# Performance work log

Measured on AMD Instinct MI355X. Metric: run time of the kernel, lower is better.

Reference implementation:

```python
import jax, jax.numpy as jnp
import numpy as np

N, D, H, B = 16384, 256, 4, 64
K_EDGE, TOP_K, NUM_HOPS = 3, 5, 2
EDGE_THRESH = 0.3
EPS = 1e-8


def setup_inputs() -> dict:
    key = jax.random.key(0)
    ks = jax.random.split(key, 32)
    g = lambda i, shape, sc=1.0: jax.random.normal(ks[i], shape, jnp.float32) * sc
    # sparse-ish symmetric adjacency (avg ~33 nonzeros/row, like a pruned memory graph)
    adj = jax.random.uniform(ks[0], (N, N), jnp.float32)
    adj = adj * (jax.random.uniform(ks[1], (N, N), jnp.float32) < 0.002)
    adj = jnp.maximum(adj, adj.T)
    return dict(
        nodes=g(2, (N, D)),
        node_values=g(3, (N,)),
        adjacency=adj,
        related_pos=g(4, (B, D)),
        query=g(5, (B, D)),
        w_in=g(6, (3 * D, D), D ** -0.5),
        b_in=jnp.zeros((3 * D,), jnp.float32),
        w_out=g(7, (D, D), D ** -0.5),
        b_out=jnp.zeros((D,), jnp.float32),
        rel_w1=g(8, (2 * D, D), (2 * D) ** -0.5),
        rel_b1=jnp.zeros((D,), jnp.float32),
        rel_w2=g(9, (D, D // 2), D ** -0.5),
        rel_b2=jnp.zeros((D // 2,), jnp.float32),
        rel_w3=g(10, (D // 2, 1), (D // 2) ** -0.5),
        rel_b3=jnp.zeros((1,), jnp.float32),
        gru_w_ih=g(11, (3 * D, D), D ** -0.5),
        gru_w_hh=g(12, (3 * D, D), D ** -0.5),
        gru_b_ih=jnp.zeros((3 * D,), jnp.float32),
        gru_b_hh=jnp.zeros((3 * D,), jnp.float32),
        node_timestamps=jax.random.randint(ks[13], (N,), 0, N),
        write_idx=jax.random.randint(ks[14], (B,), 0, N),
        total_writes=N,
    )


def _l2n(x):
    return x / (jnp.linalg.norm(x, axis=-1, keepdims=True) + EPS)


def reference(nodes, node_values, adjacency, related_pos, query,
              w_in, b_in, w_out, b_out,
              rel_w1, rel_b1, rel_w2, rel_b2, rel_w3, rel_b3,
              gru_w_ih, gru_w_hh, gru_b_ih, gru_b_hh,
              node_timestamps, write_idx, total_writes):
    b, d = query.shape
    n = nodes.shape[0]
    dh = d // H
    nodes_n = _l2n(nodes)

    # ---- write path: cosine-sim top-k edge scoring + relation-encoder MLP ----
    sims_w = _l2n(related_pos) @ nodes_n.T                      # [B,N]
    _, nbr = jax.lax.top_k(sims_w, K_EDGE)                      # [B,K]
    src = nodes[write_idx]                                      # [B,D]
    dst = nodes[nbr]                                            # [B,K,D]
    comb = jnp.concatenate(
        [jnp.broadcast_to(src[:, None, :], dst.shape), dst], -1)  # [B,K,2D]
    h = jax.nn.relu(comb @ rel_w1 + rel_b1)
    h = jax.nn.relu(h @ rel_w2 + rel_b2)
    strength = jax.nn.sigmoid(h @ rel_w3 + rel_b3)[..., 0]     # [B,K]
    same = nbr == write_idx[:, None]
    old = adjacency[write_idx[:, None], nbr]
    val = jnp.where(same, old, strength)                        # skip self-edges
    adj2 = adjacency.at[write_idx[:, None], nbr].set(val)
    adj2 = adj2.at[nbr, write_idx[:, None]].set(val)            # symmetric write

    # ---- retrieval: weighted cosine similarity + top-k seeds ----
    sims = _l2n(query) @ nodes_n.T                              # [B,N]
    recency = jnp.exp(-0.01 * (total_writes - node_timestamps).astype(jnp.float32))
    weighted = sims * jax.nn.sigmoid(node_values) * recency
    _, seed = jax.lax.top_k(weighted, TOP_K)                    # [B,TOP_K]
    visited = jnp.zeros((b, n), bool).at[jnp.arange(b)[:, None], seed].set(True)

    # ---- multi-hop graph expansion over thresholded adjacency ----
    adj_bool = (adj2 > EDGE_THRESH).astype(jnp.float32)
    for _ in range(NUM_HOPS):
        visited = visited | ((visited.astype(jnp.float32) @ adj_bool) > 0)

    # ---- masked multi-head attention: query attends to visited nodes ----
    q = (query @ w_in[:d].T + b_in[:d]).reshape(b, H, dh)
    k = (nodes @ w_in[d:2 * d].T + b_in[d:2 * d]).reshape(n, H, dh)
    v = (nodes @ w_in[2 * d:].T + b_in[2 * d:]).reshape(n, H, dh)
    scores = jnp.einsum('bhd,nhd->bhn', q, k) / np.float32(np.sqrt(dh))
    scores = jnp.where(visited[:, None, :], scores, jnp.float32(-1e9))
    attn = jax.nn.softmax(scores, axis=-1)
    ctx = jnp.einsum('bhn,nhd->bhd', attn, v).reshape(b, d)
    attended = ctx @ w_out.T + b_out                            # [B,D]

    # ---- GRUCell memory evolution: x=query, h=attended ----
    gi = query @ gru_w_ih.T + gru_b_ih
    gh = attended @ gru_w_hh.T + gru_b_hh
    i_r, i_z, i_n = jnp.split(gi, 3, -1)
    h_r, h_z, h_n = jnp.split(gh, 3, -1)
    r = jax.nn.sigmoid(i_r + h_r)
    z = jax.nn.sigmoid(i_z + h_z)
    nn_ = jnp.tanh(i_n + r * h_n)
    evolved = (1.0 - z) * nn_ + z * attended                    # [B,D]
    return evolved
```

## Files before the change

kernel.cpp:

```cpp
#include <hip/hip_runtime.h>
#include <math.h>
#include <stdint.h>

#define NN 16384
#define DD 256
#define ETH 0.3f
#define EDGE_CAP (4*1024*1024)

typedef unsigned long long u64;
typedef uint32_t u32;
typedef float f32x4 __attribute__((ext_vector_type(4)));

__global__ __launch_bounds__(256) void node_stats_k(const float* __restrict__ nodes,
    const float* __restrict__ nv, const int* __restrict__ ts, const int* __restrict__ tw,
    float* __restrict__ inv_norm, float* __restrict__ sal){
  int row = blockIdx.x*4 + (threadIdx.x>>6);
  int lane = threadIdx.x & 63;
  const float4* r4 = (const float4*)(nodes + (size_t)row*DD);
  float4 v = r4[lane];
  float s = v.x*v.x+v.y*v.y+v.z*v.z+v.w*v.w;
  #pragma unroll
  for (int o=32;o>0;o>>=1) s += __shfl_down(s,o);
  if (lane==0){
    inv_norm[row] = 1.0f/(sqrtf(s)+1e-8f);
    float x = nv[row];
    float sig = 1.0f/(1.0f+expf(-x));
    float rec = expf(-0.01f*(float)(tw[0]-ts[row]));
    sal[row] = sig*rec;
  }
}

__global__ __launch_bounds__(64) void norm_qr_k(const float* __restrict__ query,
    const float* __restrict__ related, float* __restrict__ qr){
  int blk = blockIdx.x; int lane = threadIdx.x;
  const float* src = (blk<64)? (related + (size_t)blk*DD) : (query + (size_t)(blk-64)*DD);
  float4 v = ((const float4*)src)[lane];
  float s = v.x*v.x+v.y*v.y+v.z*v.z+v.w*v.w;
  #pragma unroll
  for (int o=32;o>0;o>>=1) s += __shfl_down(s,o);
  s = __shfl(s,0);
  float inv = 1.0f/(sqrtf(s)+1e-8f);
  ((float4*)(qr + (size_t)blk*DD))[lane] = make_float4(v.x*inv,v.y*inv,v.z*inv,v.w*inv);
}

#define ACC8(r) do{ \
    accA[r].x += qs*nv0.x; accA[r].y += qs*nv0.y; accA[r].z += qs*nv0.z; accA[r].w += qs*nv0.w; \
    accB[r].x += qs*nv1.x; accB[r].y += qs*nv1.y; accB[r].z += qs*nv1.z; accB[r].w += qs*nv1.w; }while(0)

template<int RM>
__global__ __launch_bounds__(256) void gemm_smallM_k(const float* __restrict__ Qm,
    const float* __restrict__ nodes, float* __restrict__ out0, float* __restrict__ out1,
    const float* __restrict__ inv_norm, const float* __restrict__ sal, int mode){
  constexpr int M = RM*32;
  constexpr int KC = 32;
  __shared__ float qk[KC*M];
  __shared__ float ndk[KC*64];
  int t = threadIdx.x;
  int qg = t>>3, ng = t&7;
  int n0 = blockIdx.x*64;
  float4 accA[RM], accB[RM];
  #pragma unroll
  for (int r=0;r<RM;r++){ accA[r]=make_float4(0,0,0,0); accB[r]=make_float4(0,0,0,0); }
  for (int kb=0; kb<DD; kb+=KC){
    if (t < M){
      const float4* src = (const float4*)(Qm + (size_t)t*DD + kb);
      #pragma unroll
      for (int i=0;i<KC/4;i++){
        float4 w = src[i];
        qk[(i*4+0)*M+t]=w.x; qk[(i*4+1)*M+t]=w.y;
        qk[(i*4+2)*M+t]=w.z; qk[(i*4+3)*M+t]=w.w;
      }
    }
    {
      int nn = t&63, kq = t>>6;
      const float4* src = (const float4*)(nodes + (size_t)(n0+nn)*DD + kb + kq*8);
      float4 a = src[0], b = src[1];
      ndk[(kq*8+0)*64+nn]=a.x; ndk[(kq*8+1)*64+nn]=a.y; ndk[(kq*8+2)*64+nn]=a.z; ndk[(kq*8+3)*64+nn]=a.w;
      ndk[(kq*8+4)*64+nn]=b.x; ndk[(kq*8+5)*64+nn]=b.y; ndk[(kq*8+6)*64+nn]=b.z; ndk[(kq*8+7)*64+nn]=b.w;
    }
    __syncthreads();
    for (int k=0;k<KC;k++){
      float4 nv0 = *(const float4*)&ndk[k*64 + ng*8];
      float4 nv1 = *(const float4*)&ndk[k*64 + ng*8 + 4];
      float4 q0  = *(const float4*)&qk[k*M + qg*RM];
      float qs;
      qs=q0.x; ACC8(0); qs=q0.y; ACC8(1); qs=q0.z; ACC8(2); qs=q0.w; ACC8(3);
      if constexpr (RM==8){
        float4 q1 = *(const float4*)&qk[k*M + qg*RM + 4];
        qs=q1.x; ACC8(4); qs=q1.y; ACC8(5); qs=q1.z; ACC8(6); qs=q1.w; ACC8(7);
      }
    }
    __syncthreads();
  }
  int nbase = n0 + ng*8;
  float4 in0, in1, sa0, sa1;
  if (mode==0){
    in0 = *(const float4*)&inv_norm[nbase]; in1 = *(const float4*)&inv_norm[nbase+4];
    sa0 = *(const float4*)&sal[nbase];      sa1 = *(const float4*)&sal[nbase+4];
  }
  #pragma unroll
  for (int r=0;r<RM;r++){
    int row = qg*RM + r;
    float4 a = accA[r], b = accB[r];
    if (mode==0){
      float4 s0 = make_float4(a.x*in0.x, a.y*in0.y, a.z*in0.z, a.w*in0.w);
      float4 s1 = make_float4(b.x*in1.x, b.y*in1.y, b.z*in1.z, b.w*in1.w);
      if (row < 64){
        *(float4*)&out0[(size_t)row*NN + nbase]     = s0;
        *(float4*)&out0[(size_t)row*NN + nbase + 4] = s1;
      } else {
        float4 w0 = make_float4(s0.x*sa0.x, s0.y*sa0.y, s0.z*sa0.z, s0.w*sa0.w);
        float4 w1 = make_float4(s1.x*sa1.x, s1.y*sa1.y, s1.z*sa1.z, s1.w*sa1.w);
        *(float4*)&out1[(size_t)(row-64)*NN + nbase]     = w0;
        *(float4*)&out1[(size_t)(row-64)*NN + nbase + 4] = w1;
      }
    } else {
      float4 s0 = make_float4(a.x*0.125f, a.y*0.125f, a.z*0.125f, a.w*0.125f);
      float4 s1 = make_float4(b.x*0.125f, b.y*0.125f, b.z*0.125f, b.w*0.125f);
      *(float4*)&out0[(size_t)row*NN + nbase]     = s0;
      *(float4*)&out0[(size_t)row*NN + nbase + 4] = s1;
    }
  }
}

__global__ __launch_bounds__(1024) void topk_k(const float* __restrict__ src, int K,
    int* __restrict__ outIdx, u64* __restrict__ vis){
  int b = blockIdx.x, t = threadIdx.x;
  const float* row = src + (size_t)b*NN;
  __shared__ float sv[1024]; __shared__ int si[1024]; __shared__ int chosen[5];
  for (int kk=0;kk<K;kk++){
    float best = -3.0e38f; int bi = NN;
    for (int n=t;n<NN;n+=1024){
      bool skip=false;
      for (int c=0;c<kk;c++) if (chosen[c]==n) skip=true;
      if (skip) continue;
      float v = row[n];
      if (v > best){ best=v; bi=n; }
    }
    sv[t]=best; si[t]=bi;
    __syncthreads();
    for (int s=512;s>0;s>>=1){
      if (t<s){
        float v2=sv[t+s]; int i2=si[t+s];
        if (v2>sv[t] || (v2==sv[t] && i2<si[t])){ sv[t]=v2; si[t]=i2; }
      }
      __syncthreads();
    }
    if (t==0){
      chosen[kk]=si[0]; outIdx[b*K+kk]=si[0];
      if (vis) atomicOr(&vis[si[0]], 1ull<<b);
    }
    __syncthreads();
  }
}

__global__ __launch_bounds__(256) void rel_patch_k(const float* __restrict__ nodes,
    const int* __restrict__ write_idx, const int* __restrict__ nbr,
    const float* __restrict__ w1, const float* __restrict__ b1,
    const float* __restrict__ w2, const float* __restrict__ b2,
    const float* __restrict__ w3, const float* __restrict__ b3,
    u32* __restrict__ modkeys, u32* __restrict__ addkeys, int* __restrict__ ctrl,
    u32* __restrict__ rowmod){
  int b = blockIdx.x, t = threadIdx.x;
  __shared__ float comb[512], h1[256], red[128];
  int w = write_idx[b];
  for (int k=0;k<3;k++){
    int nb = nbr[b*3+k];
    comb[t]     = nodes[(size_t)w*DD + t];
    comb[256+t] = nodes[(size_t)nb*DD + t];
    __syncthreads();
    float a1 = b1[t];
    for (int i=0;i<512;i++) a1 += comb[i]*w1[(size_t)i*256 + t];
    h1[t] = a1>0.f ? a1 : 0.f;
    __syncthreads();
    if (t<128){
      float a2 = b2[t];
      for (int i=0;i<256;i++) a2 += h1[i]*w2[(size_t)i*128 + t];
      float h2 = a2>0.f ? a2 : 0.f;
      red[t] = h2*w3[t];
    }
    __syncthreads();
    for (int s=64;s>0;s>>=1){ if (t<s) red[t]+=red[t+s]; __syncthreads(); }
    if (t==0 && nb != w){
      float strength = 1.0f/(1.0f+expf(-(red[0]+b3[0])));
      u32 k1 = ((u32)w<<14)|(u32)nb, k2 = ((u32)nb<<14)|(u32)w;
      int m = atomicAdd(&ctrl[1],2);
      modkeys[m]=k1; modkeys[m+1]=k2;
      if (strength > ETH){ int a=atomicAdd(&ctrl[2],2); addkeys[a]=k1; addkeys[a+1]=k2; }
      atomicOr(&rowmod[(u32)w>>5], 1u<<((u32)w&31));
      atomicOr(&rowmod[(u32)nb>>5], 1u<<((u32)nb&31));
    }
    __syncthreads();
  }
}

#define LCAP 4096
#define GITER 8
#define ISSUE(P, GB) do{ \
  asm volatile("global_load_dwordx4 %0, %1, off" : "=v"(P##0) : "v"(a4 + tid + (size_t)((GB)+0)*stride)); \
  asm volatile("global_load_dwordx4 %0, %1, off" : "=v"(P##1) : "v"(a4 + tid + (size_t)((GB)+1)*stride)); \
  asm volatile("global_load_dwordx4 %0, %1, off" : "=v"(P##2) : "v"(a4 + tid + (size_t)((GB)+2)*stride)); \
  asm volatile("global_load_dwordx4 %0, %1, off" : "=v"(P##3) : "v"(a4 + tid + (size_t)((GB)+3)*stride)); \
  asm volatile("global_load_dwordx4 %0, %1, off" : "=v"(P##4) : "v"(a4 + tid + (size_t)((GB)+4)*stride)); \
  asm volatile("global_load_dwordx4 %0, %1, off" : "=v"(P##5) : "v"(a4 + tid + (size_t)((GB)+5)*stride)); \
  asm volatile("global_load_dwordx4 %0, %1, off" : "=v"(P##6) : "v"(a4 + tid + (size_t)((GB)+6)*stride)); \
  asm volatile("global_load_dwordx4 %0, %1, off" : "=v"(P##7) : "v"(a4 + tid + (size_t)((GB)+7)*stride)); \
}while(0)
#define PROC1(XX, GI) do{ \
  _Pragma("unroll") \
  for (int e=0;e<4;e++){ \
    if (XX[e] > ETH){ \
      size_t li = (tid + (size_t)(GI)*stride)*4 + e; \
      u32 i = (u32)(li >> 14), j = (u32)(li & 16383); \
      u32 key = (i<<14)|j; \
      bool keep = true; \
      if ((rowmod[i>>5]>>(i&31))&1u){ \
        for (int c=0;c<nm;c++) if (modkeys[c]==key){ keep=false; break; } \
      } \
      if (keep){ \
        int p = atomicAdd(&lcnt, 1); \
        if (p < LCAP) lbuf[p] = key; \
        else { int d = atomicAdd(ecnt,1); if (d < EDGE_CAP) edges[d] = key; } \
      } \
    } \
  } }while(0)
#define PROC8(P, GB) do{ \
  PROC1(P##0,(GB)+0); PROC1(P##1,(GB)+1); PROC1(P##2,(GB)+2); PROC1(P##3,(GB)+3); \
  PROC1(P##4,(GB)+4); PROC1(P##5,(GB)+5); PROC1(P##6,(GB)+6); PROC1(P##7,(GB)+7); \
}while(0)

__global__ __launch_bounds__(256) void scan_adj_k(const float* __restrict__ adj,
    const u32* __restrict__ rowmod, const u32* __restrict__ modkeys,
    const int* __restrict__ ctrl, u32* __restrict__ edges, int* __restrict__ ecnt){
  __shared__ u32 lbuf[LCAP];
  __shared__ int lcnt, gbase;
  int t = threadIdx.x;
  if (t==0) lcnt = 0;
  __syncthreads();
  int nm = ctrl[1];
  size_t tid = (size_t)blockIdx.x*256 + t;
  size_t stride = (size_t)gridDim.x*256;
  const f32x4* a4 = (const f32x4*)adj;
  const size_t total4 = (size_t)NN*NN/4;
  const int iters = (int)(total4 / stride);
  f32x4 xa0,xa1,xa2,xa3,xa4,xa5,xa6,xa7;
  f32x4 xb0,xb1,xb2,xb3,xb4,xb5,xb6,xb7;
  ISSUE(xa, 0);
  #pragma unroll 1
  for (int g=0; g<iters; g+=2*GITER){
    ISSUE(xb, g+GITER);
    asm volatile("s_waitcnt vmcnt(8)" ::: "memory");
    __builtin_amdgcn_sched_barrier(0);
    PROC8(xa, g);
    if (g + 2*GITER < iters){
      ISSUE(xa, g+2*GITER);
      asm volatile("s_waitcnt vmcnt(8)" ::: "memory");
    } else {
      asm volatile("s_waitcnt vmcnt(0)" ::: "memory");
    }
    __builtin_amdgcn_sched_barrier(0);
    PROC8(xb, g+GITER);
  }
  __syncthreads();
  int cnt = lcnt; if (cnt > LCAP) cnt = LCAP;
  if (cnt > 0){
    if (t==0) gbase = atomicAdd(ecnt, cnt);
    __syncthreads();
    int b0 = gbase;
    for (int i=t; i<cnt; i+=256){
      int d = b0 + i;
      if (d < EDGE_CAP) edges[d] = lbuf[i];
    }
  }
}

__global__ void patch_add_k(const u32* __restrict__ addkeys, const int* __restrict__ ctrl,
    u32* __restrict__ edges, int* __restrict__ ecnt){
  if (blockIdx.x==0 && threadIdx.x==0){
    int na = ctrl[2];
    int base = atomicAdd(ecnt, na);
    for (int i=0;i<na;i++) if (base+i < EDGE_CAP) edges[base+i] = addkeys[i];
  }
}

__global__ __launch_bounds__(256) void propagate_k(const u32* __restrict__ edges,
    const int* __restrict__ ecnt, const u64* __restrict__ vin, u64* __restrict__ vout){
  int n = *ecnt; if (n > EDGE_CAP) n = EDGE_CAP;
  int tid = blockIdx.x*256 + threadIdx.x;
  int stride = gridDim.x*256;
  for (int idx=tid; idx<n; idx+=stride){
    u32 key = edges[idx];
    u32 i = key>>14, j = key & 16383u;
    u64 wv = vin[i];
    if (wv) atomicOr(&vout[j], wv);
  }
}

__global__ __launch_bounds__(256) void qproj_k(const float* __restrict__ query,
    const float* __restrict__ w_in, const float* __restrict__ b_in, float* __restrict__ qproj){
  int b = blockIdx.x, o = threadIdx.x;
  float s = b_in[o];
  const float* wr = w_in + (size_t)o*256;
  const float* q = query + (size_t)b*256;
  for (int c=0;c<256;c++) s += q[c]*wr[c];
  qproj[b*256+o]=s;
}

__global__ __launch_bounds__(256) void qw_k(const float* __restrict__ qproj,
    const float* __restrict__ w_in, float* __restrict__ qW){
  int r = blockIdx.x;
  int c = threadIdx.x;
  int b = r>>2, hh = r&3;
  float s=0.f;
  for (int dh=0; dh<64; dh++)
    s += qproj[b*256 + hh*64 + dh] * w_in[(size_t)(256 + hh*64 + dh)*256 + c];
  qW[(size_t)r*256+c]=s;
}

__global__ __launch_bounds__(256) void rowstat_k(const float* __restrict__ scores,
    const u64* __restrict__ vis, float* __restrict__ m_out, float* __restrict__ is_out){
  int r = blockIdx.x; int bb = r >> 2; int t = threadIdx.x;
  const float* row = scores + (size_t)r*NN;
  float m = -3.0e38f, s = 0.f;
  for (int n=t; n<NN; n+=256){
    if ((vis[n]>>bb)&1ull){
      float v = row[n];
      if (v > m){ s = s*__expf(m - v) + 1.0f; m = v; }
      else s += __expf(v - m);
    }
  }
  __shared__ float sm[256], ss[256];
  sm[t]=m; ss[t]=s; __syncthreads();
  for (int st=128; st>0; st>>=1){
    if (t<st){
      float m2=sm[t+st], s2=ss[t+st];
      float mm = fmaxf(sm[t], m2);
      ss[t] = ss[t]*__expf(sm[t]-mm) + s2*__expf(m2-mm);
      sm[t] = mm;
    }
    __syncthreads();
  }
  if (t==0){ m_out[r] = sm[0]; is_out[r] = 1.0f/ss[0]; }
}

__global__ __launch_bounds__(256) void agg_k(const float* __restrict__ attn,
    const float* __restrict__ m_in, const float* __restrict__ is_in,
    const u64* __restrict__ vis, const float* __restrict__ nodes, float* __restrict__ partial){
  int c = blockIdx.x;
  int h = blockIdx.y;
  int t = threadIdx.x;
  int bb = t >> 2, qq = t & 3;
  __shared__ float att[64*129];
  __shared__ float smx[64], sis[64];
  if (t < 64){ smx[t] = m_in[t*4+h]; sis[t] = is_in[t*4+h]; }
  float4 acc[16];
  #pragma unroll
  for (int i=0;i<16;i++) acc[i] = make_float4(0.f,0.f,0.f,0.f);
  for (int sub=0; sub<2; sub++){
    int n0 = c*256 + sub*128;
    __syncthreads();
    for (int idx=t; idx<64*128; idx+=256){
      int rb = idx>>7, nn = idx&127;
      int node = n0 + nn;
      float raw = attn[((size_t)(rb*4+h))*NN + node];
      float p = ((vis[node]>>rb)&1ull) ? __expf(raw - smx[rb])*sis[rb] : 0.f;
      att[rb*129+nn] = p;
    }
    __syncthreads();
    for (int nn=0; nn<128; nn++){
      float a = att[bb*129+nn];
      const float4* nr = (const float4*)(nodes + ((size_t)(n0+nn))*DD + qq*64);
      #pragma unroll
      for (int i=0;i<16;i++){
        float4 x = nr[i];
        acc[i].x += a*x.x; acc[i].y += a*x.y; acc[i].z += a*x.z; acc[i].w += a*x.w;
      }
    }
  }
  float* dst = partial + (((size_t)(c*4+h)*64 + bb)*256) + qq*64;
  #pragma unroll
  for (int i=0;i<16;i++) ((float4*)dst)[i] = acc[i];
}

__global__ __launch_bounds__(256) void reduce_partial_k(const float* __restrict__ partial,
    float* __restrict__ ctxraw){
  int idx = blockIdx.x*256 + threadIdx.x;
  int d = idx & 255; int bh = idx >> 8;
  int hh = bh & 3, b = bh >> 2;
  float s=0.f;
  for (int c=0;c<64;c++) s += partial[(((size_t)c*4+hh)*64 + b)*256 + d];
  ctxraw[idx] = s;
}

__global__ __launch_bounds__(256) void ctx_k(const float* __restrict__ ctxraw,
    const float* __restrict__ w_in, const float* __restrict__ b_in, float* __restrict__ ctx){
  int b = blockIdx.x, o = threadIdx.x;
  int hh = o >> 6;
  const float* cr = ctxraw + (size_t)(b*4+hh)*256;
  const float* wr = w_in + (size_t)(512+o)*256;
  float s = b_in[512+o];
  for (int d=0; d<256; d++) s += cr[d]*wr[d];
  ctx[b*256+o] = s;
}

__global__ __launch_bounds__(256) void attended_k(const float* __restrict__ ctx,
    const float* __restrict__ w_out, const float* __restrict__ b_out, float* __restrict__ att){
  int b = blockIdx.x, o = threadIdx.x;
  const float* cr = ctx + (size_t)b*256;
  const float* wr = w_out + (size_t)o*256;
  float s = b_out[o];
  for (int c=0;c<256;c++) s += cr[c]*wr[c];
  att[b*256+o] = s;
}

__global__ __launch_bounds__(256) void gru_k(const float* __restrict__ query,
    const float* __restrict__ att, const float* __restrict__ w_ih, const float* __restrict__ w_hh,
    const float* __restrict__ b_ih, const float* __restrict__ b_hh, float* __restrict__ out){
  int b = blockIdx.x, o = threadIdx.x;
  const float* q = query + (size_t)b*256;
  const float* a = att + (size_t)b*256;
  float ir=b_ih[o], iz=b_ih[256+o], inn=b_ih[512+o];
  float hr=b_hh[o], hz=b_hh[256+o], hn=b_hh[512+o];
  for (int c=0;c<256;c++){
    float qc=q[c], ac=a[c];
    ir += qc*w_ih[(size_t)o*256+c];
    iz += qc*w_ih[(size_t)(256+o)*256+c];
    inn+= qc*w_ih[(size_t)(512+o)*256+c];
    hr += ac*w_hh[(size_t)o*256+c];
    hz += ac*w_hh[(size_t)(256+o)*256+c];
    hn += ac*w_hh[(size_t)(512+o)*256+c];
  }
  float r = 1.f/(1.f+expf(-(ir+hr)));
  float z = 1.f/(1.f+expf(-(iz+hz)));
  float nval = tanhf(inn + r*hn);
  out[b*256+o] = (1.f-z)*nval + z*a[o];
}

extern "C" void kernel_launch(void* const* d_in, const int* in_sizes, int n_in,
                              void* d_out, int out_size, void* d_ws, size_t ws_size,
                              hipStream_t stream){
  (void)in_sizes; (void)n_in; (void)out_size; (void)ws_size;
  const float* nodes     = (const float*)d_in[0];
  const float* node_vals = (const float*)d_in[1];
  const float* adjacency = (const float*)d_in[2];
  const float* related   = (const float*)d_in[3];
  const float* query     = (const float*)d_in[4];
  const float* w_in      = (const float*)d_in[5];
  const float* b_in      = (const float*)d_in[6];
  const float* w_out     = (const float*)d_in[7];
  const float* b_out     = (const float*)d_in[8];
  const float* rel_w1    = (const float*)d_in[9];
  const float* rel_b1    = (const float*)d_in[10];
  const float* rel_w2    = (const float*)d_in[11];
  const float* rel_b2    = (const float*)d_in[12];
  const float* rel_w3    = (const float*)d_in[13];
  const float* rel_b3    = (const float*)d_in[14];
  const float* gw_ih     = (const float*)d_in[15];
  const float* gw_hh     = (const float*)d_in[16];
  const float* gb_ih     = (const float*)d_in[17];
  const float* gb_hh     = (const float*)d_in[18];
  const int*   ts        = (const int*)d_in[19];
  const int*   write_idx = (const int*)d_in[20];
  const int*   tw        = (const int*)d_in[21];
  float* out = (float*)d_out;

  char* ws = (char*)d_ws;
  size_t off = 0;
  auto alloc = [&](size_t bytes)->char*{
    char* p = ws + off; off += (bytes + 255) & ~(size_t)255; return p;
  };
  float* inv_norm = (float*)alloc(NN*4);
  float* sal      = (float*)alloc(NN*4);
  float* qr       = (float*)alloc(128*DD*4);
  float* simw     = (float*)alloc((size_t)64*NN*4);
  float* wsims    = (float*)alloc((size_t)64*NN*4);
  int*   nbr      = (int*)  alloc(64*3*4);
  int*   seed     = (int*)  alloc(64*5*4);
  float* qproj    = (float*)alloc(64*256*4);
  float* qW       = (float*)alloc(256*256*4);
  float* scores   = (float*)alloc((size_t)256*NN*4);
  float* m_row    = (float*)alloc(256*4);
  float* is_row   = (float*)alloc(256*4);
  float* ctxraw   = (float*)alloc(64*4*256*4);
  float* ctx      = (float*)alloc(64*256*4);
  float* attended = (float*)alloc(64*256*4);
  u64*   V0       = (u64*)  alloc(NN*8);
  u64*   V1       = (u64*)  alloc(NN*8);
  u32*   edges    = (u32*)  alloc((size_t)EDGE_CAP*4);
  float* partial  = (float*)edges;
  int*   ctrl     = (int*)  alloc(256);
  u32*   modkeys  = (u32*)  alloc(512*4);
  u32*   addkeys  = (u32*)  alloc(512*4);
  u32*   rowmod   = (u32*)  alloc(NN/8);

  hipMemsetAsync(ctrl, 0, 256, stream);
  hipMemsetAsync(rowmod, 0, NN/8, stream);
  hipMemsetAsync(V0, 0, NN*8, stream);

  node_stats_k<<<NN/4, 256, 0, stream>>>(nodes, node_vals, ts, tw, inv_norm, sal);
  norm_qr_k<<<128, 64, 0, stream>>>(query, related, qr);
  gemm_smallM_k<4><<<NN/64, 256, 0, stream>>>(qr, nodes, simw, wsims, inv_norm, sal, 0);
  topk_k<<<64, 1024, 0, stream>>>(simw, 3, nbr, (u64*)nullptr);
  topk_k<<<64, 1024, 0, stream>>>(wsims, 5, seed, V0);
  rel_patch_k<<<64, 256, 0, stream>>>(nodes, write_idx, nbr, rel_w1, rel_b1, rel_w2, rel_b2,
                                      rel_w3, rel_b3, modkeys, addkeys, ctrl, rowmod);
  scan_adj_k<<<2048, 256, 0, stream>>>(adjacency, rowmod, modkeys, ctrl, edges, &ctrl[0]);
  patch_add_k<<<1, 64, 0, stream>>>(addkeys, ctrl, edges, &ctrl[0]);
  hipMemcpyAsync(V1, V0, NN*8, hipMemcpyDeviceToDevice, stream);
  propagate_k<<<1024, 256, 0, stream>>>(edges, &ctrl[0], V0, V1);
  hipMemcpyAsync(V0, V1, NN*8, hipMemcpyDeviceToDevice, stream);
  propagate_k<<<1024, 256, 0, stream>>>(edges, &ctrl[0], V1, V0);
  qproj_k<<<64, 256, 0, stream>>>(query, w_in, b_in, qproj);
  qw_k<<<256, 256, 0, stream>>>(qproj, w_in, qW);
  gemm_smallM_k<8><<<NN/64, 256, 0, stream>>>(qW, nodes, scores, (float*)nullptr,
                                              (const float*)nullptr, (const float*)nullptr, 1);
  rowstat_k<<<256, 256, 0, stream>>>(scores, V0, m_row, is_row);
  agg_k<<<dim3(64,4), 256, 0, stream>>>(scores, m_row, is_row, V0, nodes, partial);
  reduce_partial_k<<<256, 256, 0, stream>>>(partial, ctxraw);
  ctx_k<<<64, 256, 0, stream>>>(ctxraw, w_in, b_in, ctx);
  attended_k<<<64, 256, 0, stream>>>(ctx, w_out, b_out, attended);
  gru_k<<<64, 256, 0, stream>>>(query, attended, gw_ih, gw_hh, gb_ih, gb_hh, out);
}
```

Before: 1.472 ms.

## Split adjacency scan into ballot bitmap stream and sparse edge extraction

The fused adjacency scan becomes two kernels. The first streams the dense 1 GiB adjacency and writes a bitmask of entries above the threshold using wavefront ballots, with no per-element branching or atomics. The second walks the 32 MiB bitmask and extracts edge keys with find-first-set, applying the modified-key filter and appending to the edge list. This keeps the bandwidth-bound stream free of divergent work, at the cost of an extra kernel launch and a 32 MiB write and read that reuse the scores buffer.

Measured after the change: 1.679 ms. 1.14x slower.

```diff
diff --git a/kernel.cpp b/kernel.cpp
--- a/kernel.cpp
+++ b/kernel.cpp
@@ -194,8 +194,6 @@
   }
 }
 
-#define LCAP 4096
-#define GITER 8
 #define ISSUE(P, GB) do{ \
   asm volatile("global_load_dwordx4 %0, %1, off" : "=v"(P##0) : "v"(a4 + tid + (size_t)((GB)+0)*stride)); \
   asm volatile("global_load_dwordx4 %0, %1, off" : "=v"(P##1) : "v"(a4 + tid + (size_t)((GB)+1)*stride)); \
@@ -206,30 +204,74 @@
   asm volatile("global_load_dwordx4 %0, %1, off" : "=v"(P##6) : "v"(a4 + tid + (size_t)((GB)+6)*stride)); \
   asm volatile("global_load_dwordx4 %0, %1, off" : "=v"(P##7) : "v"(a4 + tid + (size_t)((GB)+7)*stride)); \
 }while(0)
-#define PROC1(XX, GI) do{ \
-  _Pragma("unroll") \
-  for (int e=0;e<4;e++){ \
-    if (XX[e] > ETH){ \
-      size_t li = (tid + (size_t)(GI)*stride)*4 + e; \
-      u32 i = (u32)(li >> 14), j = (u32)(li & 16383); \
-      u32 key = (i<<14)|j; \
-      bool keep = true; \
-      if ((rowmod[i>>5]>>(i&31))&1u){ \
-        for (int c=0;c<nm;c++) if (modkeys[c]==key){ keep=false; break; } \
-      } \
-      if (keep){ \
-        int p = atomicAdd(&lcnt, 1); \
-        if (p < LCAP) lbuf[p] = key; \
-        else { int d = atomicAdd(ecnt,1); if (d < EDGE_CAP) edges[d] = key; } \
-      } \
+#define BAL1(XX, GI) do{ \
+  u64 b0 = __ballot(XX[0] > ETH); \
+  u64 b1 = __ballot(XX[1] > ETH); \
+  u64 b2 = __ballot(XX[2] > ETH); \
+  u64 b3 = __ballot(XX[3] > ETH); \
+  if (lane < 4){ \
+    u64 mine = (lane==0)?b0:((lane==1)?b1:((lane==2)?b2:b3)); \
+    bm[(wtid + (size_t)(GI)*chpi)*4 + (u32)lane] = mine; \
+  } \
+}while(0)
+#define BAL8(P, GB) do{ \
+  BAL1(P##0,(GB)+0); BAL1(P##1,(GB)+1); BAL1(P##2,(GB)+2); BAL1(P##3,(GB)+3); \
+  BAL1(P##4,(GB)+4); BAL1(P##5,(GB)+5); BAL1(P##6,(GB)+6); BAL1(P##7,(GB)+7); \
+}while(0)
+
+__global__ __launch_bounds__(256) void stream_bits_k(const float* __restrict__ adj,
+    u64* __restrict__ bm){
+  int t = threadIdx.x;
+  int lane = t & 63;
+  size_t tid = (size_t)blockIdx.x*256 + t;
+  size_t stride = (size_t)gridDim.x*256;
+  size_t wtid = tid >> 6;
+  size_t chpi = stride >> 6;
+  const f32x4* a4 = (const f32x4*)adj;
+  const size_t total4 = (size_t)NN*NN/4;
+  const int iters = (int)(total4 / stride);
+  f32x4 xa0,xa1,xa2,xa3,xa4,xa5,xa6,xa7;
+  f32x4 xb0,xb1,xb2,xb3,xb4,xb5,xb6,xb7;
+  ISSUE(xa, 0);
+  #pragma unroll 1
+  for (int g=0; g<iters; g+=16){
+    ISSUE(xb, g+8);
+    asm volatile("s_waitcnt vmcnt(8)" ::: "memory");
+    __builtin_amdgcn_sched_barrier(0);
+    BAL8(xa, g);
+    if (g + 16 < iters){
+      ISSUE(xa, g+16);
+      asm volatile("s_waitcnt vmcnt(8)" ::: "memory");
+    } else {
+      asm volatile("s_waitcnt vmcnt(0)" ::: "memory");
+    }
+    __builtin_amdgcn_sched_barrier(0);
+    BAL8(xb, g+8);
+  }
+}
+
+#define LCAP 4096
+#define NCHUNK ((size_t)NN*NN/256)
+#define EXT1(WW, E) do{ \
+  u64 w_ = (WW); \
+  while (w_){ \
+    int l = __ffsll((unsigned long long)w_) - 1; w_ &= w_ - 1; \
+    size_t li = (size_t)c*256 + (size_t)l*4 + (E); \
+    u32 i = (u32)(li >> 14), j = (u32)(li & 16383); \
+    u32 key = (i<<14)|j; \
+    bool keep = true; \
+    if ((rowmod[i>>5]>>(i&31))&1u){ \
+      for (int cc=0; cc<nm; cc++) if (modkeys[cc]==key){ keep=false; break; } \
     } \
-  } }while(0)
-#define PROC8(P, GB) do{ \
-  PROC1(P##0,(GB)+0); PROC1(P##1,(GB)+1); PROC1(P##2,(GB)+2); PROC1(P##3,(GB)+3); \
-  PROC1(P##4,(GB)+4); PROC1(P##5,(GB)+5); PROC1(P##6,(GB)+6); PROC1(P##7,(GB)+7); \
+    if (keep){ \
+      int p = atomicAdd(&lcnt, 1); \
+      if (p < LCAP) lbuf[p] = key; \
+      else { int d = atomicAdd(ecnt,1); if (d < EDGE_CAP) edges[d] = key; } \
+    } \
+  } \
 }while(0)
 
-__global__ __launch_bounds__(256) void scan_adj_k(const float* __restrict__ adj,
+__global__ __launch_bounds__(256) void extract_k(const u64* __restrict__ bm,
     const u32* __restrict__ rowmod, const u32* __restrict__ modkeys,
     const int* __restrict__ ctrl, u32* __restrict__ edges, int* __restrict__ ecnt){
   __shared__ u32 lbuf[LCAP];
@@ -240,26 +282,9 @@
   int nm = ctrl[1];
   size_t tid = (size_t)blockIdx.x*256 + t;
   size_t stride = (size_t)gridDim.x*256;
-  const f32x4* a4 = (const f32x4*)adj;
-  const size_t total4 = (size_t)NN*NN/4;
-  const int iters = (int)(total4 / stride);
-  f32x4 xa0,xa1,xa2,xa3,xa4,xa5,xa6,xa7;
-  f32x4 xb0,xb1,xb2,xb3,xb4,xb5,xb6,xb7;
-  ISSUE(xa, 0);
-  #pragma unroll 1
-  for (int g=0; g<iters; g+=2*GITER){
-    ISSUE(xb, g+GITER);
-    asm volatile("s_waitcnt vmcnt(8)" ::: "memory");
-    __builtin_amdgcn_sched_barrier(0);
-    PROC8(xa, g);
-    if (g + 2*GITER < iters){
-      ISSUE(xa, g+2*GITER);
-      asm volatile("s_waitcnt vmcnt(8)" ::: "memory");
-    } else {
-      asm volatile("s_waitcnt vmcnt(0)" ::: "memory");
-    }
-    __builtin_amdgcn_sched_barrier(0);
-    PROC8(xb, g+GITER);
+  for (size_t c = tid; c < NCHUNK; c += stride){
+    u64 w0 = bm[c*4+0], w1 = bm[c*4+1], w2 = bm[c*4+2], w3 = bm[c*4+3];
+    EXT1(w0, 0); EXT1(w1, 1); EXT1(w2, 2); EXT1(w3, 3);
   }
   __syncthreads();
   int cnt = lcnt; if (cnt > LCAP) cnt = LCAP;
@@ -478,7 +503,9 @@
   int*   seed     = (int*)  alloc(64*5*4);
   float* qproj    = (float*)alloc(64*256*4);
   float* qW       = (float*)alloc(256*256*4);
-  float* scores   = (float*)alloc((size_t)256*NN*4);
+  char*  big      = alloc((size_t)32*1024*1024);
+  u64*   bm       = (u64*)big;
+  float* scores   = (float*)big;
   float* m_row    = (float*)alloc(256*4);
   float* is_row   = (float*)alloc(256*4);
   float* ctxraw   = (float*)alloc(64*4*256*4);
@@ -504,7 +531,8 @@
   topk_k<<<64, 1024, 0, stream>>>(wsims, 5, seed, V0);
   rel_patch_k<<<64, 256, 0, stream>>>(nodes, write_idx, nbr, rel_w1, rel_b1, rel_w2, rel_b2,
                                       rel_w3, rel_b3, modkeys, addkeys, ctrl, rowmod);
-  scan_adj_k<<<2048, 256, 0, stream>>>(adjacency, rowmod, modkeys, ctrl, edges, &ctrl[0]);
+  stream_bits_k<<<2048, 256, 0, stream>>>(adjacency, bm);
+  extract_k<<<1024, 256, 0, stream>>>(bm, rowmod, modkeys, ctrl, edges, &ctrl[0]);
   patch_add_k<<<1, 64, 0, stream>>>(addkeys, ctrl, edges, &ctrl[0]);
   hipMemcpyAsync(V1, V0, NN*8, hipMemcpyDeviceToDevice, stream);
   propagate_k<<<1024, 256, 0, stream>>>(edges, &ctrl[0], V0, V1);
```

## Single-pass top-k and fuse softmax stats into attention aggregation

Applied to the files above, without the earlier changes.

Top-k now keeps a per-thread sorted list of five candidates and merges the lists in one shared-memory tree reduction, replacing K full passes over the row. The separate row-statistics kernel is removed: agg_k computes a local max and sum for each tile, the reduce kernel merges the tiles online with rescaling, and nodes whose attention weight is zero are skipped. This removes one full read of the score matrix and cuts the top-k passes to one. In exchange agg_k uses a larger shared-memory tile, which may lower occupancy, and the tree merge puts more sequential insertion work on each thread.

After: 1.265 ms (median of 3 runs). 1.16x faster.

```diff
diff --git a/kernel.cpp b/kernel.cpp
--- a/kernel.cpp
+++ b/kernel.cpp
@@ -123,34 +123,51 @@
   }
 }
 
+#define TK_INS(cv,ci) do{ \
+  if (cv>v4 || (cv==v4 && ci<i4)){ \
+    if (cv>v0 || (cv==v0 && ci<i0)){ v4=v3;i4=i3; v3=v2;i3=i2; v2=v1;i2=i1; v1=v0;i1=i0; v0=cv;i0=ci; } \
+    else if (cv>v1 || (cv==v1 && ci<i1)){ v4=v3;i4=i3; v3=v2;i3=i2; v2=v1;i2=i1; v1=cv;i1=ci; } \
+    else if (cv>v2 || (cv==v2 && ci<i2)){ v4=v3;i4=i3; v3=v2;i3=i2; v2=cv;i2=ci; } \
+    else if (cv>v3 || (cv==v3 && ci<i3)){ v4=v3;i4=i3; v3=cv;i3=ci; } \
+    else { v4=cv;i4=ci; } \
+  } \
+}while(0)
+
 __global__ __launch_bounds__(1024) void topk_k(const float* __restrict__ src, int K,
     int* __restrict__ outIdx, u64* __restrict__ vis){
   int b = blockIdx.x, t = threadIdx.x;
   const float* row = src + (size_t)b*NN;
-  __shared__ float sv[1024]; __shared__ int si[1024]; __shared__ int chosen[5];
-  for (int kk=0;kk<K;kk++){
-    float best = -3.0e38f; int bi = NN;
-    for (int n=t;n<NN;n+=1024){
-      bool skip=false;
-      for (int c=0;c<kk;c++) if (chosen[c]==n) skip=true;
-      if (skip) continue;
-      float v = row[n];
-      if (v > best){ best=v; bi=n; }
-    }
-    sv[t]=best; si[t]=bi;
-    __syncthreads();
-    for (int s=512;s>0;s>>=1){
-      if (t<s){
-        float v2=sv[t+s]; int i2=si[t+s];
-        if (v2>sv[t] || (v2==sv[t] && i2<si[t])){ sv[t]=v2; si[t]=i2; }
+  float v0=-3.0e38f,v1=-3.0e38f,v2=-3.0e38f,v3=-3.0e38f,v4=-3.0e38f;
+  int i0=0x7fffffff,i1=0x7fffffff,i2=0x7fffffff,i3=0x7fffffff,i4=0x7fffffff;
+  for (int n=t; n<NN; n+=1024){
+    float cv = row[n];
+    TK_INS(cv, n);
+  }
+  __shared__ float sv[1024*5];
+  __shared__ int   si[1024*5];
+  sv[t*5+0]=v0; si[t*5+0]=i0; sv[t*5+1]=v1; si[t*5+1]=i1;
+  sv[t*5+2]=v2; si[t*5+2]=i2; sv[t*5+3]=v3; si[t*5+3]=i3;
+  sv[t*5+4]=v4; si[t*5+4]=i4;
+  __syncthreads();
+  for (int s=512; s>0; s>>=1){
+    if (t < s){
+      #pragma unroll
+      for (int k=0;k<5;k++){
+        float cv = sv[(t+s)*5+k]; int ci = si[(t+s)*5+k];
+        TK_INS(cv, ci);
       }
-      __syncthreads();
-    }
-    if (t==0){
-      chosen[kk]=si[0]; outIdx[b*K+kk]=si[0];
-      if (vis) atomicOr(&vis[si[0]], 1ull<<b);
-    }
-    __syncthreads();
+      sv[t*5+0]=v0; si[t*5+0]=i0; sv[t*5+1]=v1; si[t*5+1]=i1;
+      sv[t*5+2]=v2; si[t*5+2]=i2; sv[t*5+3]=v3; si[t*5+3]=i3;
+      sv[t*5+4]=v4; si[t*5+4]=i4;
+    }
+    __syncthreads();
+  }
+  if (t==0){
+    int idxs[5] = {i0,i1,i2,i3,i4};
+    for (int kk=0; kk<K; kk++){
+      outIdx[b*K+kk] = idxs[kk];
+      if (vis) atomicOr(&vis[idxs[kk]], 1ull<<b);
+    }
   }
 }
 
@@ -317,58 +334,42 @@
   qW[(size_t)r*256+c]=s;
 }
 
-__global__ __launch_bounds__(256) void rowstat_k(const float* __restrict__ scores,
-    const u64* __restrict__ vis, float* __restrict__ m_out, float* __restrict__ is_out){
-  int r = blockIdx.x; int bb = r >> 2; int t = threadIdx.x;
-  const float* row = scores + (size_t)r*NN;
-  float m = -3.0e38f, s = 0.f;
-  for (int n=t; n<NN; n+=256){
-    if ((vis[n]>>bb)&1ull){
-      float v = row[n];
-      if (v > m){ s = s*__expf(m - v) + 1.0f; m = v; }
-      else s += __expf(v - m);
-    }
-  }
-  __shared__ float sm[256], ss[256];
-  sm[t]=m; ss[t]=s; __syncthreads();
-  for (int st=128; st>0; st>>=1){
-    if (t<st){
-      float m2=sm[t+st], s2=ss[t+st];
-      float mm = fmaxf(sm[t], m2);
-      ss[t] = ss[t]*__expf(sm[t]-mm) + s2*__expf(m2-mm);
-      sm[t] = mm;
-    }
-    __syncthreads();
-  }
-  if (t==0){ m_out[r] = sm[0]; is_out[r] = 1.0f/ss[0]; }
-}
-
-__global__ __launch_bounds__(256) void agg_k(const float* __restrict__ attn,
-    const float* __restrict__ m_in, const float* __restrict__ is_in,
-    const u64* __restrict__ vis, const float* __restrict__ nodes, float* __restrict__ partial){
+__global__ __launch_bounds__(256) void agg_k(const float* __restrict__ scores,
+    const u64* __restrict__ vis, const float* __restrict__ nodes,
+    float* __restrict__ partial, float* __restrict__ m_arr, float* __restrict__ s_arr){
   int c = blockIdx.x;
   int h = blockIdx.y;
   int t = threadIdx.x;
   int bb = t >> 2, qq = t & 3;
-  __shared__ float att[64*129];
-  __shared__ float smx[64], sis[64];
-  if (t < 64){ smx[t] = m_in[t*4+h]; sis[t] = is_in[t*4+h]; }
+  __shared__ float att[64][257];
+  int n0 = c*256;
+  for (int idx=t; idx<64*256; idx+=256){
+    int rb = idx>>8, nn = idx&255;
+    int node = n0 + nn;
+    float raw = scores[((size_t)(rb*4+h))*NN + node];
+    att[rb][nn] = ((vis[node]>>rb)&1ull) ? raw : -3.0e38f;
+  }
+  __syncthreads();
+  float m = -3.0e38f;
+  for (int j=0;j<64;j++) m = fmaxf(m, att[bb][qq*64+j]);
+  m = fmaxf(m, __shfl_xor(m,1));
+  m = fmaxf(m, __shfl_xor(m,2));
+  float s = 0.f;
+  for (int j=0;j<64;j++){ float v = att[bb][qq*64+j]; if (v > -1.0e37f) s += __expf(v-m); }
+  s += __shfl_xor(s,1);
+  s += __shfl_xor(s,2);
+  __syncthreads();
+  for (int j=0;j<64;j++){
+    float v = att[bb][qq*64+j];
+    att[bb][qq*64+j] = (v > -1.0e37f) ? __expf(v-m) : 0.f;
+  }
+  __syncthreads();
   float4 acc[16];
   #pragma unroll
   for (int i=0;i<16;i++) acc[i] = make_float4(0.f,0.f,0.f,0.f);
-  for (int sub=0; sub<2; sub++){
-    int n0 = c*256 + sub*128;
-    __syncthreads();
-    for (int idx=t; idx<64*128; idx+=256){
-      int rb = idx>>7, nn = idx&127;
-      int node = n0 + nn;
-      float raw = attn[((size_t)(rb*4+h))*NN + node];
-      float p = ((vis[node]>>rb)&1ull) ? __expf(raw - smx[rb])*sis[rb] : 0.f;
-      att[rb*129+nn] = p;
-    }
-    __syncthreads();
-    for (int nn=0; nn<128; nn++){
-      float a = att[bb*129+nn];
+  for (int nn=0; nn<256; nn++){
+    float a = att[bb][nn];
+    if (a != 0.f){
       const float4* nr = (const float4*)(nodes + ((size_t)(n0+nn))*DD + qq*64);
       #pragma unroll
       for (int i=0;i<16;i++){
@@ -380,16 +381,35 @@
   float* dst = partial + (((size_t)(c*4+h)*64 + bb)*256) + qq*64;
   #pragma unroll
   for (int i=0;i<16;i++) ((float4*)dst)[i] = acc[i];
+  if (qq==0){
+    m_arr[(c*4+h)*64 + bb] = m;
+    s_arr[(c*4+h)*64 + bb] = s;
+  }
 }
 
 __global__ __launch_bounds__(256) void reduce_partial_k(const float* __restrict__ partial,
+    const float* __restrict__ m_arr, const float* __restrict__ s_arr,
     float* __restrict__ ctxraw){
   int idx = blockIdx.x*256 + threadIdx.x;
   int d = idx & 255; int bh = idx >> 8;
   int hh = bh & 3, b = bh >> 2;
-  float s=0.f;
-  for (int c=0;c<64;c++) s += partial[(((size_t)c*4+hh)*64 + b)*256 + d];
-  ctxraw[idx] = s;
+  float M = -3.0e38f, S = 0.f, acc = 0.f;
+  for (int c=0;c<64;c++){
+    int rb = (c*4+hh)*64 + b;
+    float mc = m_arr[rb], sc = s_arr[rb];
+    float pv = partial[((size_t)rb)*256 + d];
+    if (mc > M){
+      float w = __expf(M - mc);
+      acc = acc*w + pv;
+      S   = S*w + sc;
+      M   = mc;
+    } else {
+      float w = __expf(mc - M);
+      acc += pv*w;
+      S   += sc*w;
+    }
+  }
+  ctxraw[idx] = acc / S;
 }
 
 __global__ __launch_bounds__(256) void ctx_k(const float* __restrict__ ctxraw,
@@ -479,8 +499,8 @@
   float* qproj    = (float*)alloc(64*256*4);
   float* qW       = (float*)alloc(256*256*4);
   float* scores   = (float*)alloc((size_t)256*NN*4);
-  float* m_row    = (float*)alloc(256*4);
-  float* is_row   = (float*)alloc(256*4);
+  float* m_arr    = (float*)alloc(64*4*64*4);
+  float* s_arr    = (float*)alloc(64*4*64*4);
   float* ctxraw   = (float*)alloc(64*4*256*4);
   float* ctx      = (float*)alloc(64*256*4);
   float* attended = (float*)alloc(64*256*4);
@@ -514,9 +534,8 @@
   qw_k<<<256, 256, 0, stream>>>(qproj, w_in, qW);
   gemm_smallM_k<8><<<NN/64, 256, 0, stream>>>(qW, nodes, scores, (float*)nullptr,
                                               (const float*)nullptr, (const float*)nullptr, 1);
-  rowstat_k<<<256, 256, 0, stream>>>(scores, V0, m_row, is_row);
-  agg_k<<<dim3(64,4), 256, 0, stream>>>(scores, m_row, is_row, V0, nodes, partial);
-  reduce_partial_k<<<256, 256, 0, stream>>>(partial, ctxraw);
+  agg_k<<<dim3(64,4), 256, 0, stream>>>(scores, V0, nodes, partial, m_arr, s_arr);
+  reduce_partial_k<<<256, 256, 0, stream>>>(partial, m_arr, s_arr, ctxraw);
   ctx_k<<<64, 256, 0, stream>>>(ctxraw, w_in, b_in, ctx);
   attended_k<<<64, 256, 0, stream>>>(ctx, w_out, b_out, attended);
   gru_k<<<64, 256, 0, stream>>>(query, attended, gw_ih, gw_hh, gb_ih, gb_hh, out);
```
